# Kernel tuning notes

Hardware: AMD Instinct MI355X
Metric: run time of the kernel (lower is better)

## Reference

```python
import jax, jax.numpy as jnp
import numpy as np

N_NODES = 100000
K_HOPS = 10
ALPHA = 0.1


def gcn_conv(x, src, dst, W, b, num_nodes):
    # GCNConv: linear first (cheaper: out_dim small), then D^-1/2 (A+I) D^-1/2 aggregation
    h = x @ W  # [N, out]
    deg = jax.ops.segment_sum(jnp.ones_like(dst, dtype=h.dtype), dst, num_segments=num_nodes)
    dinv = jnp.where(deg > 0, jax.lax.rsqrt(deg), 0.0)
    norm = dinv[src] * dinv[dst]  # [E]
    msg = h[src] * norm[:, None]
    out = jax.ops.segment_sum(msg, dst, num_segments=num_nodes)
    return out + b


def _with_self_loops(edge_index, num_nodes):
    loops = jnp.arange(num_nodes, dtype=edge_index.dtype)
    src = jnp.concatenate([edge_index[0], loops])
    dst = jnp.concatenate([edge_index[1], loops])
    return src, dst


def setup_inputs() -> dict:
    key = jax.random.key(0)
    ks = jax.random.split(key, 8)
    n_feat, hidden, n_cls, n_edges = 512, 16, 7, 3200000
    x = jax.random.normal(ks[0], (N_NODES, n_feat), dtype=jnp.float32)
    edge_index = jax.random.randint(ks[1], (2, n_edges), 0, N_NODES, dtype=jnp.int64)
    W1 = jax.random.normal(ks[2], (n_feat, hidden), dtype=jnp.float32) * 0.05
    b1 = jnp.zeros((hidden,), dtype=jnp.float32)
    Wl = jax.random.normal(ks[3], (hidden, hidden), dtype=jnp.float32) * 0.25
    bl = jnp.zeros((hidden,), dtype=jnp.float32)
    W2 = jax.random.normal(ks[4], (hidden, n_cls), dtype=jnp.float32) * 0.25
    b2 = jnp.zeros((n_cls,), dtype=jnp.float32)
    return {"x": x, "edge_index": edge_index, "W1": W1, "b1": b1, "Wl": Wl, "bl": bl, "W2": W2, "b2": b2}


def reference(x, edge_index, W1, b1, Wl, bl, W2, b2):
    src, dst = _with_self_loops(edge_index, N_NODES)
    h = jax.nn.relu(gcn_conv(x, src, dst, W1, b1, N_NODES))
    def body(h, _):
        h = ALPHA * jax.nn.relu(h @ Wl + bl) + (1.0 - ALPHA) * h
        return h, None
    h, _ = jax.lax.scan(body, h, None, length=K_HOPS)
    out = gcn_conv(h, src, dst, W2, b2, N_NODES)
    return jax.nn.log_softmax(out, axis=1)
```

## Files before the change

### kernel.cpp

```cpp
#include <hip/hip_runtime.h>
#include <math.h>

#define N_NODES 100000
#define N_EDGES 3200000
#define F_IN    512
#define HID     16
#define NCLS    7
#define ALPHA   0.1f
#define K_HOPS  10

#define SHIFT   7
#define BWIDTH  128
#define NBUCK   ((N_NODES + BWIDTH - 1) / BWIDTH)
#define CHUNK   4096
#define BIN_T   512
#define EPT     (CHUNK / BIN_T)
#define A3_BLOCKS ((N_EDGES + CHUNK - 1) / CHUNK)

#define OFF_BCNT    0u
#define OFF_BSTART  1024u
#define OFF_BCUR    2048u
#define OFF_RP      3072u
#define OFF_DINV    103424u
#define OFF_COL     203776u
#define OFF_BINNED  3403776u
#define OFF_H0      6603776u
#define OFF_H1      8203776u
#define OFF_Z       9803776u

__global__ void k_bhist(const int* __restrict__ dst, int* __restrict__ bcnt) {
    __shared__ int h[NBUCK];
    int tid = threadIdx.x;
    for (int i = tid; i < NBUCK; i += 256) h[i] = 0;
    __syncthreads();
    for (int e = blockIdx.x * 256 + tid; e < N_EDGES; e += gridDim.x * 256)
        atomicAdd(&h[dst[e] >> SHIFT], 1);
    __syncthreads();
    for (int i = tid; i < NBUCK; i += 256) {
        int v = h[i];
        if (v) atomicAdd(&bcnt[i], v);
    }
}

__global__ void k_bscan(const int* __restrict__ bcnt, int* __restrict__ bstart,
                        int* __restrict__ bcur) {
    __shared__ int s[1024];
    int tid = threadIdx.x;
    int v = (tid < NBUCK) ? bcnt[tid] : 0;
    s[tid] = v;
    __syncthreads();
    for (int off = 1; off < 1024; off <<= 1) {
        int t = (tid >= off) ? s[tid - off] : 0;
        __syncthreads();
        s[tid] += t;
        __syncthreads();
    }
    if (tid < NBUCK) {
        int ex = s[tid] - v;
        bstart[tid] = ex;
        bcur[tid] = ex;
    }
    if (tid == 0) bstart[NBUCK] = N_EDGES;
}

__global__ void __launch_bounds__(BIN_T)
k_bin(const int* __restrict__ src, const int* __restrict__ dst,
      int* __restrict__ bcur, unsigned int* __restrict__ binned) {
    __shared__ int ha[NBUCK];
    __shared__ int gbase[NBUCK];
    __shared__ int lcur[NBUCK];
    int tid = threadIdx.x;
    int e0 = blockIdx.x * CHUNK;
    int e1 = e0 + CHUNK;
    if (e1 > N_EDGES) e1 = N_EDGES;
    for (int i = tid; i < NBUCK; i += BIN_T) ha[i] = 0;
    __syncthreads();
    int dloc[EPT];
#pragma unroll
    for (int i = 0; i < EPT; i++) {
        int e = e0 + tid + i * BIN_T;
        dloc[i] = (e < e1) ? dst[e] : -1;
        if (dloc[i] >= 0) atomicAdd(&ha[dloc[i] >> SHIFT], 1);
    }
    __syncthreads();
    for (int s = tid; s < NBUCK; s += BIN_T) {
        int c = ha[s];
        lcur[s] = 0;
        gbase[s] = c ? atomicAdd(&bcur[s], c) : 0;
    }
    __syncthreads();
#pragma unroll
    for (int i = 0; i < EPT; i++) {
        int d = dloc[i];
        if (d >= 0) {
            int e = e0 + tid + i * BIN_T;
            int bk = d >> SHIFT;
            int idx = atomicAdd(&lcur[bk], 1);
            binned[gbase[bk] + idx] =
                ((unsigned int)(d & (BWIDTH - 1)) << 17) | (unsigned int)src[e];
        }
    }
}

__global__ void __launch_bounds__(512)
k_csr(const unsigned int* __restrict__ binned, const int* __restrict__ bstart,
      int* __restrict__ rp, float* __restrict__ dinv, int* __restrict__ col) {
    __shared__ int cnt[BWIDTH];
    __shared__ int s[BWIDTH];
    __shared__ int cur[BWIDTH];
    int tid = threadIdx.x;
    int b = blockIdx.x;
    int base = b << SHIFT;
    int e0 = bstart[b], e1 = bstart[b + 1];
    if (tid < BWIDTH) cnt[tid] = 0;
    __syncthreads();
    for (int e = e0 + tid; e < e1; e += 512)
        atomicAdd(&cnt[binned[e] >> 17], 1);
    __syncthreads();
    int v = 0;
    if (tid < BWIDTH) { v = cnt[tid]; s[tid] = v; }
    __syncthreads();
    for (int off = 1; off < BWIDTH; off <<= 1) {
        int t = 0;
        if (tid < BWIDTH && tid >= off) t = s[tid - off];
        __syncthreads();
        if (tid < BWIDTH) s[tid] += t;
        __syncthreads();
    }
    if (tid < BWIDTH) {
        int ex = s[tid] - v;
        cur[tid] = ex;
        int node = base + tid;
        if (node < N_NODES) {
            rp[node] = e0 + ex;
            dinv[node] = rsqrtf((float)(v + 1));
        }
    }
    if (b == 0 && tid == 0) rp[N_NODES] = N_EDGES;
    __syncthreads();
    for (int e = e0 + tid; e < e1; e += 512) {
        unsigned int w = binned[e];
        int ln = (int)(w >> 17);
        int p = atomicAdd(&cur[ln], 1);
        col[e0 + p] = (int)(w & 0x1FFFFu);
    }
}

#define XW_ROWS 64
#define XW_KT   32
#define XW_S    36
#define XW_NT   (F_IN / XW_KT)
__global__ void k_xw1(const float* __restrict__ x, const float* __restrict__ W,
                      const float* __restrict__ dinv, float* __restrict__ h0s) {
    __shared__ float xT[2][XW_ROWS * XW_S];
    int tid = threadIdx.x;
    int rowBase = blockIdx.x * XW_ROWS;

    int rf0 = tid >> 3, kq = tid & 7;
    int rf1 = rf0 + 32;
    bool v0 = (rowBase + rf0) < N_NODES;
    bool v1 = (rowBase + rf1) < N_NODES;
    const float4* xrow0 = (const float4*)(x + (size_t)(rowBase + rf0) * F_IN);
    const float4* xrow1 = (const float4*)(x + (size_t)(rowBase + rf1) * F_IN);

    int r  = tid & 63;
    int cg = __builtin_amdgcn_readfirstlane(tid >> 6);
    const float4* W4 = (const float4*)W;

    float4 zero4 = make_float4(0.f, 0.f, 0.f, 0.f);
    float4 acc = zero4;
    float4 ld0 = v0 ? xrow0[kq] : zero4;
    float4 ld1 = v1 ? xrow1[kq] : zero4;

    for (int kt = 0; kt < XW_NT; kt++) {
        float* xb = xT[kt & 1];
        *(float4*)&xb[rf0 * XW_S + kq * 4] = ld0;
        *(float4*)&xb[rf1 * XW_S + kq * 4] = ld1;
        if (kt + 1 < XW_NT) {
            ld0 = v0 ? xrow0[(kt + 1) * 8 + kq] : zero4;
            ld1 = v1 ? xrow1[(kt + 1) * 8 + kq] : zero4;
        }
        __syncthreads();
        const float* xr = &xb[r * XW_S];
#pragma unroll
        for (int k8 = 0; k8 < 8; k8++) {
            float4 xv = *(const float4*)&xr[k8 * 4];
            float4 w0 = W4[(kt * XW_KT + k8 * 4 + 0) * 4 + cg];
            acc.x += xv.x * w0.x; acc.y += xv.x * w0.y;
            acc.z += xv.x * w0.z; acc.w += xv.x * w0.w;
            float4 w1 = W4[(kt * XW_KT + k8 * 4 + 1) * 4 + cg];
            acc.x += xv.y * w1.x; acc.y += xv.y * w1.y;
            acc.z += xv.y * w1.z; acc.w += xv.y * w1.w;
            float4 w2 = W4[(kt * XW_KT + k8 * 4 + 2) * 4 + cg];
            acc.x += xv.z * w2.x; acc.y += xv.z * w2.y;
            acc.z += xv.z * w2.z; acc.w += xv.z * w2.w;
            float4 w3 = W4[(kt * XW_KT + k8 * 4 + 3) * 4 + cg];
            acc.x += xv.w * w3.x; acc.y += xv.w * w3.y;
            acc.z += xv.w * w3.z; acc.w += xv.w * w3.w;
        }
        __syncthreads();
    }
    int node = rowBase + r;
    if (node < N_NODES) {
        float dv = dinv[node];
        float4 o;
        o.x = dv * acc.x; o.y = dv * acc.y; o.z = dv * acc.z; o.w = dv * acc.w;
        ((float4*)h0s)[(size_t)node * 4 + cg] = o;
    }
}

__global__ void k_agg1(const float* __restrict__ h0s, const int* __restrict__ rp,
                       const int* __restrict__ col, const float* __restrict__ dinv,
                       const float* __restrict__ b1, float* __restrict__ h1) {
    int node = (blockIdx.x * blockDim.x + threadIdx.x) >> 6;
    if (node >= N_NODES) return;
    int lane = threadIdx.x & 63;
    int c = lane & 15, eo = lane >> 4;
    int e0 = rp[node], e1 = rp[node + 1];
    float acc = 0.f;
    int e = e0 + eo;
    for (; e + 12 < e1; e += 16) {
        int c0 = col[e];
        int c1 = col[e + 4];
        int c2 = col[e + 8];
        int c3 = col[e + 12];
        float v0 = h0s[(size_t)c0 * HID + c];
        float v1 = h0s[(size_t)c1 * HID + c];
        float v2 = h0s[(size_t)c2 * HID + c];
        float v3 = h0s[(size_t)c3 * HID + c];
        acc += v0;
        acc += v1;
        acc += v2;
        acc += v3;
    }
    for (; e + 4 < e1; e += 8) {
        int c0 = col[e];
        int c1 = col[e + 4];
        float v0 = h0s[(size_t)c0 * HID + c];
        float v1 = h0s[(size_t)c1 * HID + c];
        acc += v0;
        acc += v1;
    }
    if (e < e1) acc += h0s[(size_t)col[e] * HID + c];
    acc += __shfl_xor(acc, 16);
    acc += __shfl_xor(acc, 32);
    float o = dinv[node] * (acc + h0s[(size_t)node * HID + c]) + b1[c];
    if (eo == 0) h1[(size_t)node * HID + c] = fmaxf(o, 0.f);
}

__global__ void k_hops(const float* __restrict__ h1, const float* __restrict__ Wl,
                       const float* __restrict__ bl, const float* __restrict__ W2,
                       const float* __restrict__ dinv, float* __restrict__ zs) {
    int node = blockIdx.x * blockDim.x + threadIdx.x;
    if (node >= N_NODES) return;
    float h[HID];
    const float4* h4 = (const float4*)(h1 + (size_t)node * HID);
#pragma unroll
    for (int q = 0; q < HID / 4; q++) {
        float4 v = h4[q];
        h[q * 4 + 0] = v.x; h[q * 4 + 1] = v.y;
        h[q * 4 + 2] = v.z; h[q * 4 + 3] = v.w;
    }
    for (int it = 0; it < K_HOPS; it++) {
        float tm[HID];
#pragma unroll
        for (int c = 0; c < HID; c++) tm[c] = bl[c];
#pragma unroll
        for (int k = 0; k < HID; k++) {
            float hk = h[k];
#pragma unroll
            for (int c = 0; c < HID; c++) tm[c] += hk * Wl[k * HID + c];
        }
#pragma unroll
        for (int c = 0; c < HID; c++)
            h[c] = ALPHA * fmaxf(tm[c], 0.f) + (1.f - ALPHA) * h[c];
    }
    float dv = dinv[node];
    float zz[8];
#pragma unroll
    for (int c = 0; c < 8; c++) zz[c] = 0.f;
#pragma unroll
    for (int k = 0; k < HID; k++) {
        float hk = h[k];
#pragma unroll
        for (int c = 0; c < NCLS; c++) zz[c] += hk * W2[k * NCLS + c];
    }
    float4* z4 = (float4*)(zs + (size_t)node * 8);
    float4 v0, v1;
    v0.x = dv * zz[0]; v0.y = dv * zz[1]; v0.z = dv * zz[2]; v0.w = dv * zz[3];
    v1.x = dv * zz[4]; v1.y = dv * zz[5]; v1.z = dv * zz[6]; v1.w = 0.f;
    z4[0] = v0; z4[1] = v1;
}

__global__ void k_agg2(const float* __restrict__ zs, const int* __restrict__ rp,
                       const int* __restrict__ col, const float* __restrict__ dinv,
                       const float* __restrict__ b2, float* __restrict__ out) {
    int node = (blockIdx.x * blockDim.x + threadIdx.x) >> 6;
    if (node >= N_NODES) return;
    int lane = threadIdx.x & 63;
    int c = lane & 7, eo = lane >> 3;
    int e0 = rp[node], e1 = rp[node + 1];
    float acc = 0.f;
    int e = e0 + eo;
    for (; e + 24 < e1; e += 32) {
        int c0 = col[e];
        int c1 = col[e + 8];
        int c2 = col[e + 16];
        int c3 = col[e + 24];
        float v0 = zs[(size_t)c0 * 8 + c];
        float v1 = zs[(size_t)c1 * 8 + c];
        float v2 = zs[(size_t)c2 * 8 + c];
        float v3 = zs[(size_t)c3 * 8 + c];
        acc += v0;
        acc += v1;
        acc += v2;
        acc += v3;
    }
    for (; e + 8 < e1; e += 16) {
        int c0 = col[e];
        int c1 = col[e + 8];
        float v0 = zs[(size_t)c0 * 8 + c];
        float v1 = zs[(size_t)c1 * 8 + c];
        acc += v0;
        acc += v1;
    }
    if (e < e1) acc += zs[(size_t)col[e] * 8 + c];
    acc += __shfl_xor(acc, 8);
    acc += __shfl_xor(acc, 16);
    acc += __shfl_xor(acc, 32);
    float o = dinv[node] * (acc + zs[(size_t)node * 8 + c]) + ((c < NCLS) ? b2[c] : 0.f);
    float val = (c < NCLS) ? o : -INFINITY;
    float m = val;
    m = fmaxf(m, __shfl_xor(m, 1));
    m = fmaxf(m, __shfl_xor(m, 2));
    m = fmaxf(m, __shfl_xor(m, 4));
    float ex = (c < NCLS) ? expf(o - m) : 0.f;
    float ss = ex;
    ss += __shfl_xor(ss, 1);
    ss += __shfl_xor(ss, 2);
    ss += __shfl_xor(ss, 4);
    if (eo == 0 && c < NCLS) out[(size_t)node * NCLS + c] = o - m - logf(ss);
}

extern "C" void kernel_launch(void* const* d_in, const int* in_sizes, int n_in,
                              void* d_out, int out_size, void* d_ws, size_t ws_size,
                              hipStream_t stream) {
    const float* x  = (const float*)d_in[0];
    const int*   ei = (const int*)d_in[1];
    const float* W1 = (const float*)d_in[2];
    const float* b1 = (const float*)d_in[3];
    const float* Wl = (const float*)d_in[4];
    const float* bl = (const float*)d_in[5];
    const float* W2 = (const float*)d_in[6];
    const float* b2 = (const float*)d_in[7];
    float* out = (float*)d_out;

    int*   wsI = (int*)d_ws;
    float* wsF = (float*)d_ws;
    int*          bcnt   = wsI + OFF_BCNT;
    int*          bstart = wsI + OFF_BSTART;
    int*          bcur   = wsI + OFF_BCUR;
    int*          rp     = wsI + OFF_RP;
    float*        dinv   = wsF + OFF_DINV;
    int*          col    = wsI + OFF_COL;
    unsigned int* binned = (unsigned int*)(wsI + OFF_BINNED);
    float*        h0s    = wsF + OFF_H0;
    float*        h1     = wsF + OFF_H1;
    float*        zs     = wsF + OFF_Z;

    const int* src = ei;
    const int* dst = ei + N_EDGES;

    hipMemsetAsync(bcnt, 0, NBUCK * sizeof(int), stream);

    k_bhist<<<1024, 256, 0, stream>>>(dst, bcnt);
    k_bscan<<<1, 1024, 0, stream>>>(bcnt, bstart, bcur);
    k_bin<<<A3_BLOCKS, BIN_T, 0, stream>>>(src, dst, bcur, binned);
    k_csr<<<NBUCK, 512, 0, stream>>>(binned, bstart, rp, dinv, col);
    k_xw1<<<(N_NODES + XW_ROWS - 1) / XW_ROWS, 256, 0, stream>>>(x, W1, dinv, h0s);
    k_agg1<<<(N_NODES * 64 + 255) / 256, 256, 0, stream>>>(h0s, rp, col, dinv, b1, h1);
    k_hops<<<(N_NODES + 255) / 256, 256, 0, stream>>>(h1, Wl, bl, W2, dinv, zs);
    k_agg2<<<(N_NODES * 64 + 255) / 256, 256, 0, stream>>>(zs, rp, col, dinv, b2, out);
}
```

Before: 568.0 us.

## Fuse all stages into one persistent kernel with grid-wide barriers

Merges the eight launches (histogram, scan, binning, CSR build, XW1, two aggregations, hops) into a single persistent kernel of 1024 blocks. Stages are separated by a software grid barrier built on global atomics and spin-waiting. The goal is to remove per-launch overhead and idle tails between the small kernels. The cost is barrier latency and grid-stride loops in place of full grids, plus a deadlock risk if the 1024 blocks cannot all be resident at once.

```diff
diff --git a/kernel.cpp b/kernel.cpp
--- a/kernel.cpp
+++ b/kernel.cpp
@@ -11,335 +11,375 @@
 
 #define SHIFT   7
 #define BWIDTH  128
-#define NBUCK   ((N_NODES + BWIDTH - 1) / BWIDTH)
-#define CHUNK   4096
-#define BIN_T   512
-#define EPT     (CHUNK / BIN_T)
-#define A3_BLOCKS ((N_EDGES + CHUNK - 1) / CHUNK)
-
-#define OFF_BCNT    0u
-#define OFF_BSTART  1024u
-#define OFF_BCUR    2048u
-#define OFF_RP      3072u
-#define OFF_DINV    103424u
-#define OFF_COL     203776u
-#define OFF_BINNED  3403776u
-#define OFF_H0      6603776u
-#define OFF_H1      8203776u
-#define OFF_Z       9803776u
-
-__global__ void k_bhist(const int* __restrict__ dst, int* __restrict__ bcnt) {
-    __shared__ int h[NBUCK];
-    int tid = threadIdx.x;
-    for (int i = tid; i < NBUCK; i += 256) h[i] = 0;
-    __syncthreads();
-    for (int e = blockIdx.x * 256 + tid; e < N_EDGES; e += gridDim.x * 256)
-        atomicAdd(&h[dst[e] >> SHIFT], 1);
-    __syncthreads();
-    for (int i = tid; i < NBUCK; i += 256) {
-        int v = h[i];
-        if (v) atomicAdd(&bcnt[i], v);
-    }
-}
-
-__global__ void k_bscan(const int* __restrict__ bcnt, int* __restrict__ bstart,
-                        int* __restrict__ bcur) {
-    __shared__ int s[1024];
-    int tid = threadIdx.x;
-    int v = (tid < NBUCK) ? bcnt[tid] : 0;
-    s[tid] = v;
-    __syncthreads();
-    for (int off = 1; off < 1024; off <<= 1) {
-        int t = (tid >= off) ? s[tid - off] : 0;
-        __syncthreads();
-        s[tid] += t;
-        __syncthreads();
-    }
-    if (tid < NBUCK) {
-        int ex = s[tid] - v;
-        bstart[tid] = ex;
-        bcur[tid] = ex;
-    }
-    if (tid == 0) bstart[NBUCK] = N_EDGES;
-}
-
-__global__ void __launch_bounds__(BIN_T)
-k_bin(const int* __restrict__ src, const int* __restrict__ dst,
-      int* __restrict__ bcur, unsigned int* __restrict__ binned) {
-    __shared__ int ha[NBUCK];
-    __shared__ int gbase[NBUCK];
-    __shared__ int lcur[NBUCK];
-    int tid = threadIdx.x;
-    int e0 = blockIdx.x * CHUNK;
-    int e1 = e0 + CHUNK;
-    if (e1 > N_EDGES) e1 = N_EDGES;
-    for (int i = tid; i < NBUCK; i += BIN_T) ha[i] = 0;
-    __syncthreads();
-    int dloc[EPT];
-#pragma unroll
-    for (int i = 0; i < EPT; i++) {
-        int e = e0 + tid + i * BIN_T;
-        dloc[i] = (e < e1) ? dst[e] : -1;
-        if (dloc[i] >= 0) atomicAdd(&ha[dloc[i] >> SHIFT], 1);
-    }
-    __syncthreads();
-    for (int s = tid; s < NBUCK; s += BIN_T) {
-        int c = ha[s];
-        lcur[s] = 0;
-        gbase[s] = c ? atomicAdd(&bcur[s], c) : 0;
-    }
-    __syncthreads();
-#pragma unroll
-    for (int i = 0; i < EPT; i++) {
-        int d = dloc[i];
-        if (d >= 0) {
-            int e = e0 + tid + i * BIN_T;
-            int bk = d >> SHIFT;
-            int idx = atomicAdd(&lcur[bk], 1);
-            binned[gbase[bk] + idx] =
-                ((unsigned int)(d & (BWIDTH - 1)) << 17) | (unsigned int)src[e];
-        }
-    }
-}
-
-__global__ void __launch_bounds__(512)
-k_csr(const unsigned int* __restrict__ binned, const int* __restrict__ bstart,
-      int* __restrict__ rp, float* __restrict__ dinv, int* __restrict__ col) {
-    __shared__ int cnt[BWIDTH];
-    __shared__ int s[BWIDTH];
-    __shared__ int cur[BWIDTH];
-    int tid = threadIdx.x;
-    int b = blockIdx.x;
-    int base = b << SHIFT;
-    int e0 = bstart[b], e1 = bstart[b + 1];
-    if (tid < BWIDTH) cnt[tid] = 0;
-    __syncthreads();
-    for (int e = e0 + tid; e < e1; e += 512)
-        atomicAdd(&cnt[binned[e] >> 17], 1);
-    __syncthreads();
-    int v = 0;
-    if (tid < BWIDTH) { v = cnt[tid]; s[tid] = v; }
-    __syncthreads();
-    for (int off = 1; off < BWIDTH; off <<= 1) {
-        int t = 0;
-        if (tid < BWIDTH && tid >= off) t = s[tid - off];
-        __syncthreads();
-        if (tid < BWIDTH) s[tid] += t;
-        __syncthreads();
-    }
-    if (tid < BWIDTH) {
-        int ex = s[tid] - v;
-        cur[tid] = ex;
-        int node = base + tid;
-        if (node < N_NODES) {
-            rp[node] = e0 + ex;
-            dinv[node] = rsqrtf((float)(v + 1));
-        }
-    }
-    if (b == 0 && tid == 0) rp[N_NODES] = N_EDGES;
-    __syncthreads();
-    for (int e = e0 + tid; e < e1; e += 512) {
-        unsigned int w = binned[e];
-        int ln = (int)(w >> 17);
-        int p = atomicAdd(&cur[ln], 1);
-        col[e0 + p] = (int)(w & 0x1FFFFu);
-    }
-}
+#define NBUCK   782
+#define CHUNK   2048
+#define EPT     8
+#define NCHUNK  ((N_EDGES + CHUNK - 1) / CHUNK)
+
+#define NB      1024
+#define BT      256
+#define NWAVES  (NB * (BT / 64))
+
+#define OFF_BAR     0u
+#define OFF_BCNT    1024u
+#define OFF_BSTART  2048u
+#define OFF_BCUR    3072u
+#define OFF_RP      4096u
+#define OFF_DINV    104448u
+#define OFF_COL     204800u
+#define OFF_BINNED  3404800u
+#define OFF_H0      6604800u
+#define OFF_H1      8204800u
+#define OFF_Z       9804800u
 
 #define XW_ROWS 64
 #define XW_KT   32
 #define XW_S    36
 #define XW_NT   (F_IN / XW_KT)
-__global__ void k_xw1(const float* __restrict__ x, const float* __restrict__ W,
-                      const float* __restrict__ dinv, float* __restrict__ h0s) {
-    __shared__ float xT[2][XW_ROWS * XW_S];
+#define XW_TILES ((N_NODES + XW_ROWS - 1) / XW_ROWS)
+
+__device__ __forceinline__ void gsync(int* bar, int idx) {
+    __syncthreads();
+    if (threadIdx.x == 0) {
+        __threadfence();
+        atomicAdd(&bar[idx], 1);
+        while (__hip_atomic_load(&bar[idx], __ATOMIC_RELAXED,
+                                 __HIP_MEMORY_SCOPE_AGENT) < NB)
+            __builtin_amdgcn_s_sleep(2);
+    }
+    __syncthreads();
+    __threadfence();
+}
+
+__global__ void __launch_bounds__(BT, 4)
+k_fused(const float* __restrict__ x, const int* __restrict__ src,
+        const int* __restrict__ dst,
+        const float* __restrict__ W1, const float* __restrict__ b1,
+        const float* __restrict__ Wl, const float* __restrict__ bl,
+        const float* __restrict__ W2, const float* __restrict__ b2,
+        int* __restrict__ bar, int* __restrict__ bcnt,
+        int* __restrict__ bstart, int* __restrict__ bcur,
+        int* __restrict__ rp, float* __restrict__ dinv,
+        int* __restrict__ col, unsigned int* __restrict__ binned,
+        float* __restrict__ h0s, float* __restrict__ h1,
+        float* __restrict__ zs, float* __restrict__ out) {
+    __shared__ __align__(16) int smem[4608];
     int tid = threadIdx.x;
-    int rowBase = blockIdx.x * XW_ROWS;
-
-    int rf0 = tid >> 3, kq = tid & 7;
-    int rf1 = rf0 + 32;
-    bool v0 = (rowBase + rf0) < N_NODES;
-    bool v1 = (rowBase + rf1) < N_NODES;
-    const float4* xrow0 = (const float4*)(x + (size_t)(rowBase + rf0) * F_IN);
-    const float4* xrow1 = (const float4*)(x + (size_t)(rowBase + rf1) * F_IN);
-
-    int r  = tid & 63;
-    int cg = __builtin_amdgcn_readfirstlane(tid >> 6);
-    const float4* W4 = (const float4*)W;
-
-    float4 zero4 = make_float4(0.f, 0.f, 0.f, 0.f);
-    float4 acc = zero4;
-    float4 ld0 = v0 ? xrow0[kq] : zero4;
-    float4 ld1 = v1 ? xrow1[kq] : zero4;
-
-    for (int kt = 0; kt < XW_NT; kt++) {
-        float* xb = xT[kt & 1];
-        *(float4*)&xb[rf0 * XW_S + kq * 4] = ld0;
-        *(float4*)&xb[rf1 * XW_S + kq * 4] = ld1;
-        if (kt + 1 < XW_NT) {
-            ld0 = v0 ? xrow0[(kt + 1) * 8 + kq] : zero4;
-            ld1 = v1 ? xrow1[(kt + 1) * 8 + kq] : zero4;
-        }
+
+    {
+        int* h = smem;
+        for (int i = tid; i < NBUCK; i += BT) h[i] = 0;
         __syncthreads();
-        const float* xr = &xb[r * XW_S];
-#pragma unroll
-        for (int k8 = 0; k8 < 8; k8++) {
-            float4 xv = *(const float4*)&xr[k8 * 4];
-            float4 w0 = W4[(kt * XW_KT + k8 * 4 + 0) * 4 + cg];
-            acc.x += xv.x * w0.x; acc.y += xv.x * w0.y;
-            acc.z += xv.x * w0.z; acc.w += xv.x * w0.w;
-            float4 w1 = W4[(kt * XW_KT + k8 * 4 + 1) * 4 + cg];
-            acc.x += xv.y * w1.x; acc.y += xv.y * w1.y;
-            acc.z += xv.y * w1.z; acc.w += xv.y * w1.w;
-            float4 w2 = W4[(kt * XW_KT + k8 * 4 + 2) * 4 + cg];
-            acc.x += xv.z * w2.x; acc.y += xv.z * w2.y;
-            acc.z += xv.z * w2.z; acc.w += xv.z * w2.w;
-            float4 w3 = W4[(kt * XW_KT + k8 * 4 + 3) * 4 + cg];
-            acc.x += xv.w * w3.x; acc.y += xv.w * w3.y;
-            acc.z += xv.w * w3.z; acc.w += xv.w * w3.w;
-        }
+        for (int e = blockIdx.x * BT + tid; e < N_EDGES; e += NB * BT)
+            atomicAdd(&h[dst[e] >> SHIFT], 1);
         __syncthreads();
-    }
-    int node = rowBase + r;
-    if (node < N_NODES) {
-        float dv = dinv[node];
-        float4 o;
-        o.x = dv * acc.x; o.y = dv * acc.y; o.z = dv * acc.z; o.w = dv * acc.w;
-        ((float4*)h0s)[(size_t)node * 4 + cg] = o;
-    }
-}
-
-__global__ void k_agg1(const float* __restrict__ h0s, const int* __restrict__ rp,
-                       const int* __restrict__ col, const float* __restrict__ dinv,
-                       const float* __restrict__ b1, float* __restrict__ h1) {
-    int node = (blockIdx.x * blockDim.x + threadIdx.x) >> 6;
-    if (node >= N_NODES) return;
-    int lane = threadIdx.x & 63;
-    int c = lane & 15, eo = lane >> 4;
-    int e0 = rp[node], e1 = rp[node + 1];
-    float acc = 0.f;
-    int e = e0 + eo;
-    for (; e + 12 < e1; e += 16) {
-        int c0 = col[e];
-        int c1 = col[e + 4];
-        int c2 = col[e + 8];
-        int c3 = col[e + 12];
-        float v0 = h0s[(size_t)c0 * HID + c];
-        float v1 = h0s[(size_t)c1 * HID + c];
-        float v2 = h0s[(size_t)c2 * HID + c];
-        float v3 = h0s[(size_t)c3 * HID + c];
-        acc += v0;
-        acc += v1;
-        acc += v2;
-        acc += v3;
-    }
-    for (; e + 4 < e1; e += 8) {
-        int c0 = col[e];
-        int c1 = col[e + 4];
-        float v0 = h0s[(size_t)c0 * HID + c];
-        float v1 = h0s[(size_t)c1 * HID + c];
-        acc += v0;
-        acc += v1;
-    }
-    if (e < e1) acc += h0s[(size_t)col[e] * HID + c];
-    acc += __shfl_xor(acc, 16);
-    acc += __shfl_xor(acc, 32);
-    float o = dinv[node] * (acc + h0s[(size_t)node * HID + c]) + b1[c];
-    if (eo == 0) h1[(size_t)node * HID + c] = fmaxf(o, 0.f);
-}
-
-__global__ void k_hops(const float* __restrict__ h1, const float* __restrict__ Wl,
-                       const float* __restrict__ bl, const float* __restrict__ W2,
-                       const float* __restrict__ dinv, float* __restrict__ zs) {
-    int node = blockIdx.x * blockDim.x + threadIdx.x;
-    if (node >= N_NODES) return;
-    float h[HID];
-    const float4* h4 = (const float4*)(h1 + (size_t)node * HID);
-#pragma unroll
-    for (int q = 0; q < HID / 4; q++) {
-        float4 v = h4[q];
-        h[q * 4 + 0] = v.x; h[q * 4 + 1] = v.y;
-        h[q * 4 + 2] = v.z; h[q * 4 + 3] = v.w;
-    }
-    for (int it = 0; it < K_HOPS; it++) {
-        float tm[HID];
-#pragma unroll
-        for (int c = 0; c < HID; c++) tm[c] = bl[c];
-#pragma unroll
-        for (int k = 0; k < HID; k++) {
-            float hk = h[k];
-#pragma unroll
-            for (int c = 0; c < HID; c++) tm[c] += hk * Wl[k * HID + c];
-        }
-#pragma unroll
-        for (int c = 0; c < HID; c++)
-            h[c] = ALPHA * fmaxf(tm[c], 0.f) + (1.f - ALPHA) * h[c];
-    }
-    float dv = dinv[node];
-    float zz[8];
-#pragma unroll
-    for (int c = 0; c < 8; c++) zz[c] = 0.f;
-#pragma unroll
-    for (int k = 0; k < HID; k++) {
-        float hk = h[k];
-#pragma unroll
-        for (int c = 0; c < NCLS; c++) zz[c] += hk * W2[k * NCLS + c];
-    }
-    float4* z4 = (float4*)(zs + (size_t)node * 8);
-    float4 v0, v1;
-    v0.x = dv * zz[0]; v0.y = dv * zz[1]; v0.z = dv * zz[2]; v0.w = dv * zz[3];
-    v1.x = dv * zz[4]; v1.y = dv * zz[5]; v1.z = dv * zz[6]; v1.w = 0.f;
-    z4[0] = v0; z4[1] = v1;
-}
-
-__global__ void k_agg2(const float* __restrict__ zs, const int* __restrict__ rp,
-                       const int* __restrict__ col, const float* __restrict__ dinv,
-                       const float* __restrict__ b2, float* __restrict__ out) {
-    int node = (blockIdx.x * blockDim.x + threadIdx.x) >> 6;
-    if (node >= N_NODES) return;
-    int lane = threadIdx.x & 63;
-    int c = lane & 7, eo = lane >> 3;
-    int e0 = rp[node], e1 = rp[node + 1];
-    float acc = 0.f;
-    int e = e0 + eo;
-    for (; e + 24 < e1; e += 32) {
-        int c0 = col[e];
-        int c1 = col[e + 8];
-        int c2 = col[e + 16];
-        int c3 = col[e + 24];
-        float v0 = zs[(size_t)c0 * 8 + c];
-        float v1 = zs[(size_t)c1 * 8 + c];
-        float v2 = zs[(size_t)c2 * 8 + c];
-        float v3 = zs[(size_t)c3 * 8 + c];
-        acc += v0;
-        acc += v1;
-        acc += v2;
-        acc += v3;
-    }
-    for (; e + 8 < e1; e += 16) {
-        int c0 = col[e];
-        int c1 = col[e + 8];
-        float v0 = zs[(size_t)c0 * 8 + c];
-        float v1 = zs[(size_t)c1 * 8 + c];
-        acc += v0;
-        acc += v1;
-    }
-    if (e < e1) acc += zs[(size_t)col[e] * 8 + c];
-    acc += __shfl_xor(acc, 8);
-    acc += __shfl_xor(acc, 16);
-    acc += __shfl_xor(acc, 32);
-    float o = dinv[node] * (acc + zs[(size_t)node * 8 + c]) + ((c < NCLS) ? b2[c] : 0.f);
-    float val = (c < NCLS) ? o : -INFINITY;
-    float m = val;
-    m = fmaxf(m, __shfl_xor(m, 1));
-    m = fmaxf(m, __shfl_xor(m, 2));
-    m = fmaxf(m, __shfl_xor(m, 4));
-    float ex = (c < NCLS) ? expf(o - m) : 0.f;
-    float ss = ex;
-    ss += __shfl_xor(ss, 1);
-    ss += __shfl_xor(ss, 2);
-    ss += __shfl_xor(ss, 4);
-    if (eo == 0 && c < NCLS) out[(size_t)node * NCLS + c] = o - m - logf(ss);
+        for (int i = tid; i < NBUCK; i += BT) {
+            int v = h[i];
+            if (v) atomicAdd(&bcnt[i], v);
+        }
+    }
+    gsync(bar, 0);
+
+    if (blockIdx.x == 0) {
+        int* s0 = smem;
+        int* s1 = smem + 1024;
+        for (int j = tid; j < 1024; j += BT) s0[j] = (j < NBUCK) ? bcnt[j] : 0;
+        __syncthreads();
+        int cur = 0;
+        for (int off = 1; off < 1024; off <<= 1) {
+            int* a = cur ? s1 : s0;
+            int* b = cur ? s0 : s1;
+            for (int j = tid; j < 1024; j += BT)
+                b[j] = a[j] + ((j >= off) ? a[j - off] : 0);
+            __syncthreads();
+            cur ^= 1;
+        }
+        int* a = cur ? s1 : s0;
+        for (int j = tid; j < 1024; j += BT) {
+            if (j < NBUCK) {
+                int ex = a[j] - bcnt[j];
+                bstart[j] = ex;
+                bcur[j] = ex;
+            }
+        }
+        if (tid == 0) bstart[NBUCK] = N_EDGES;
+    }
+    gsync(bar, 1);
+
+    {
+        int* ha    = smem;
+        int* gbase = smem + NBUCK;
+        int* lcur  = smem + 2 * NBUCK;
+        for (int ch = blockIdx.x; ch < NCHUNK; ch += NB) {
+            int e0 = ch * CHUNK;
+            int e1 = e0 + CHUNK;
+            if (e1 > N_EDGES) e1 = N_EDGES;
+            for (int i = tid; i < NBUCK; i += BT) ha[i] = 0;
+            __syncthreads();
+            int dloc[EPT];
+#pragma unroll
+            for (int i = 0; i < EPT; i++) {
+                int e = e0 + tid + i * BT;
+                dloc[i] = (e < e1) ? dst[e] : -1;
+                if (dloc[i] >= 0) atomicAdd(&ha[dloc[i] >> SHIFT], 1);
+            }
+            __syncthreads();
+            for (int s = tid; s < NBUCK; s += BT) {
+                int c = ha[s];
+                lcur[s] = 0;
+                gbase[s] = c ? atomicAdd(&bcur[s], c) : 0;
+            }
+            __syncthreads();
+#pragma unroll
+            for (int i = 0; i < EPT; i++) {
+                int d = dloc[i];
+                if (d >= 0) {
+                    int e = e0 + tid + i * BT;
+                    int bk = d >> SHIFT;
+                    int idx = atomicAdd(&lcur[bk], 1);
+                    binned[gbase[bk] + idx] =
+                        ((unsigned int)(d & (BWIDTH - 1)) << 17) | (unsigned int)src[e];
+                }
+            }
+            __syncthreads();
+        }
+    }
+    gsync(bar, 2);
+
+    {
+        int* cnt = smem;
+        int* s   = smem + BWIDTH;
+        int* cur = smem + 2 * BWIDTH;
+        for (int b = blockIdx.x; b < NBUCK; b += NB) {
+            int base = b << SHIFT;
+            int e0 = bstart[b], e1 = bstart[b + 1];
+            if (tid < BWIDTH) cnt[tid] = 0;
+            __syncthreads();
+            for (int e = e0 + tid; e < e1; e += BT)
+                atomicAdd(&cnt[binned[e] >> 17], 1);
+            __syncthreads();
+            int v = 0;
+            if (tid < BWIDTH) { v = cnt[tid]; s[tid] = v; }
+            __syncthreads();
+            for (int off = 1; off < BWIDTH; off <<= 1) {
+                int t = 0;
+                if (tid < BWIDTH && tid >= off) t = s[tid - off];
+                __syncthreads();
+                if (tid < BWIDTH) s[tid] += t;
+                __syncthreads();
+            }
+            if (tid < BWIDTH) {
+                int ex = s[tid] - v;
+                cur[tid] = ex;
+                int node = base + tid;
+                if (node < N_NODES) {
+                    rp[node] = e0 + ex;
+                    dinv[node] = rsqrtf((float)(v + 1));
+                }
+            }
+            if (b == 0 && tid == 0) rp[N_NODES] = N_EDGES;
+            __syncthreads();
+            for (int e = e0 + tid; e < e1; e += BT) {
+                unsigned int w = binned[e];
+                int ln = (int)(w >> 17);
+                int p = atomicAdd(&cur[ln], 1);
+                col[e0 + p] = (int)(w & 0x1FFFFu);
+            }
+            __syncthreads();
+        }
+    }
+    gsync(bar, 3);
+
+    {
+        float* xT = (float*)smem;
+        int rf0 = tid >> 3, kq = tid & 7;
+        int rf1 = rf0 + 32;
+        int r  = tid & 63;
+        int cg = __builtin_amdgcn_readfirstlane(tid >> 6);
+        const float4* W4 = (const float4*)W1;
+        float4 zero4 = make_float4(0.f, 0.f, 0.f, 0.f);
+
+        for (int t = blockIdx.x; t < XW_TILES; t += NB) {
+            int rowBase = t * XW_ROWS;
+            bool v0 = (rowBase + rf0) < N_NODES;
+            bool v1 = (rowBase + rf1) < N_NODES;
+            const float4* xrow0 = (const float4*)(x + (size_t)(rowBase + rf0) * F_IN);
+            const float4* xrow1 = (const float4*)(x + (size_t)(rowBase + rf1) * F_IN);
+            float4 acc = zero4;
+            float4 ld0 = v0 ? xrow0[kq] : zero4;
+            float4 ld1 = v1 ? xrow1[kq] : zero4;
+
+            for (int kt = 0; kt < XW_NT; kt++) {
+                float* xb = xT + (kt & 1) * (XW_ROWS * XW_S);
+                *(float4*)&xb[rf0 * XW_S + kq * 4] = ld0;
+                *(float4*)&xb[rf1 * XW_S + kq * 4] = ld1;
+                if (kt + 1 < XW_NT) {
+                    ld0 = v0 ? xrow0[(kt + 1) * 8 + kq] : zero4;
+                    ld1 = v1 ? xrow1[(kt + 1) * 8 + kq] : zero4;
+                }
+                __syncthreads();
+                const float* xr = &xb[r * XW_S];
+#pragma unroll
+                for (int k8 = 0; k8 < 8; k8++) {
+                    float4 xv = *(const float4*)&xr[k8 * 4];
+                    float4 w0 = W4[(kt * XW_KT + k8 * 4 + 0) * 4 + cg];
+                    acc.x += xv.x * w0.x; acc.y += xv.x * w0.y;
+                    acc.z += xv.x * w0.z; acc.w += xv.x * w0.w;
+                    float4 w1 = W4[(kt * XW_KT + k8 * 4 + 1) * 4 + cg];
+                    acc.x += xv.y * w1.x; acc.y += xv.y * w1.y;
+                    acc.z += xv.y * w1.z; acc.w += xv.y * w1.w;
+                    float4 w2 = W4[(kt * XW_KT + k8 * 4 + 2) * 4 + cg];
+                    acc.x += xv.z * w2.x; acc.y += xv.z * w2.y;
+                    acc.z += xv.z * w2.z; acc.w += xv.z * w2.w;
+                    float4 w3 = W4[(kt * XW_KT + k8 * 4 + 3) * 4 + cg];
+                    acc.x += xv.w * w3.x; acc.y += xv.w * w3.y;
+                    acc.z += xv.w * w3.z; acc.w += xv.w * w3.w;
+                }
+                __syncthreads();
+            }
+            int node = rowBase + r;
+            if (node < N_NODES) {
+                float dv = dinv[node];
+                float4 o;
+                o.x = dv * acc.x; o.y = dv * acc.y;
+                o.z = dv * acc.z; o.w = dv * acc.w;
+                ((float4*)h0s)[(size_t)node * 4 + cg] = o;
+            }
+        }
+    }
+    gsync(bar, 4);
+
+    {
+        int wid = blockIdx.x * (BT / 64) + (tid >> 6);
+        int lane = tid & 63;
+        int c = lane & 15, eo = lane >> 4;
+        for (int node = wid; node < N_NODES; node += NWAVES) {
+            int e0 = rp[node], e1 = rp[node + 1];
+            float acc = 0.f;
+            int e = e0 + eo;
+            for (; e + 12 < e1; e += 16) {
+                int c0 = col[e];
+                int c1 = col[e + 4];
+                int c2 = col[e + 8];
+                int c3 = col[e + 12];
+                float v0 = h0s[(size_t)c0 * HID + c];
+                float v1 = h0s[(size_t)c1 * HID + c];
+                float v2 = h0s[(size_t)c2 * HID + c];
+                float v3 = h0s[(size_t)c3 * HID + c];
+                acc += v0;
+                acc += v1;
+                acc += v2;
+                acc += v3;
+            }
+            for (; e + 4 < e1; e += 8) {
+                int c0 = col[e];
+                int c1 = col[e + 4];
+                float v0 = h0s[(size_t)c0 * HID + c];
+                float v1 = h0s[(size_t)c1 * HID + c];
+                acc += v0;
+                acc += v1;
+            }
+            if (e < e1) acc += h0s[(size_t)col[e] * HID + c];
+            acc += __shfl_xor(acc, 16);
+            acc += __shfl_xor(acc, 32);
+            float o = dinv[node] * (acc + h0s[(size_t)node * HID + c]) + b1[c];
+            if (eo == 0) h1[(size_t)node * HID + c] = fmaxf(o, 0.f);
+        }
+    }
+    gsync(bar, 5);
+
+    {
+        for (int node = blockIdx.x * BT + tid; node < N_NODES; node += NB * BT) {
+            float h[HID];
+            const float4* h4 = (const float4*)(h1 + (size_t)node * HID);
+#pragma unroll
+            for (int q = 0; q < HID / 4; q++) {
+                float4 v = h4[q];
+                h[q * 4 + 0] = v.x; h[q * 4 + 1] = v.y;
+                h[q * 4 + 2] = v.z; h[q * 4 + 3] = v.w;
+            }
+            for (int it = 0; it < K_HOPS; it++) {
+                float tm[HID];
+#pragma unroll
+                for (int cc = 0; cc < HID; cc++) tm[cc] = bl[cc];
+#pragma unroll
+                for (int k = 0; k < HID; k++) {
+                    float hk = h[k];
+#pragma unroll
+                    for (int cc = 0; cc < HID; cc++) tm[cc] += hk * Wl[k * HID + cc];
+                }
+#pragma unroll
+                for (int cc = 0; cc < HID; cc++)
+                    h[cc] = ALPHA * fmaxf(tm[cc], 0.f) + (1.f - ALPHA) * h[cc];
+            }
+            float dv = dinv[node];
+            float zz[8];
+#pragma unroll
+            for (int cc = 0; cc < 8; cc++) zz[cc] = 0.f;
+#pragma unroll
+            for (int k = 0; k < HID; k++) {
+                float hk = h[k];
+#pragma unroll
+                for (int cc = 0; cc < NCLS; cc++) zz[cc] += hk * W2[k * NCLS + cc];
+            }
+            float4* z4 = (float4*)(zs + (size_t)node * 8);
+            float4 v0, v1;
+            v0.x = dv * zz[0]; v0.y = dv * zz[1]; v0.z = dv * zz[2]; v0.w = dv * zz[3];
+            v1.x = dv * zz[4]; v1.y = dv * zz[5]; v1.z = dv * zz[6]; v1.w = 0.f;
+            z4[0] = v0; z4[1] = v1;
+        }
+    }
+    gsync(bar, 6);
+
+    {
+        int wid = blockIdx.x * (BT / 64) + (tid >> 6);
+        int lane = tid & 63;
+        int c = lane & 7, eo = lane >> 3;
+        for (int node = wid; node < N_NODES; node += NWAVES) {
+            int e0 = rp[node], e1 = rp[node + 1];
+            float acc = 0.f;
+            int e = e0 + eo;
+            for (; e + 24 < e1; e += 32) {
+                int c0 = col[e];
+                int c1 = col[e + 8];
+                int c2 = col[e + 16];
+                int c3 = col[e + 24];
+                float v0 = zs[(size_t)c0 * 8 + c];
+                float v1 = zs[(size_t)c1 * 8 + c];
+                float v2 = zs[(size_t)c2 * 8 + c];
+                float v3 = zs[(size_t)c3 * 8 + c];
+                acc += v0;
+                acc += v1;
+                acc += v2;
+                acc += v3;
+            }
+            for (; e + 8 < e1; e += 16) {
+                int c0 = col[e];
+                int c1 = col[e + 8];
+                float v0 = zs[(size_t)c0 * 8 + c];
+                float v1 = zs[(size_t)c1 * 8 + c];
+                acc += v0;
+                acc += v1;
+            }
+            if (e < e1) acc += zs[(size_t)col[e] * 8 + c];
+            acc += __shfl_xor(acc, 8);
+            acc += __shfl_xor(acc, 16);
+            acc += __shfl_xor(acc, 32);
+            float o = dinv[node] * (acc + zs[(size_t)node * 8 + c])
+                      + ((c < NCLS) ? b2[c] : 0.f);
+            float val = (c < NCLS) ? o : -INFINITY;
+            float m = val;
+            m = fmaxf(m, __shfl_xor(m, 1));
+            m = fmaxf(m, __shfl_xor(m, 2));
+            m = fmaxf(m, __shfl_xor(m, 4));
+            float ex = (c < NCLS) ? expf(o - m) : 0.f;
+            float ss = ex;
+            ss += __shfl_xor(ss, 1);
+            ss += __shfl_xor(ss, 2);
+            ss += __shfl_xor(ss, 4);
+            if (eo == 0 && c < NCLS) out[(size_t)node * NCLS + c] = o - m - logf(ss);
+        }
+    }
 }
 
 extern "C" void kernel_launch(void* const* d_in, const int* in_sizes, int n_in,
@@ -357,6 +397,7 @@
 
     int*   wsI = (int*)d_ws;
     float* wsF = (float*)d_ws;
+    int*          bar    = wsI + OFF_BAR;
     int*          bcnt   = wsI + OFF_BCNT;
     int*          bstart = wsI + OFF_BSTART;
     int*          bcur   = wsI + OFF_BCUR;
@@ -371,14 +412,9 @@
     const int* src = ei;
     const int* dst = ei + N_EDGES;
 
-    hipMemsetAsync(bcnt, 0, NBUCK * sizeof(int), stream);
-
-    k_bhist<<<1024, 256, 0, stream>>>(dst, bcnt);
-    k_bscan<<<1, 1024, 0, stream>>>(bcnt, bstart, bcur);
-    k_bin<<<A3_BLOCKS, BIN_T, 0, stream>>>(src, dst, bcur, binned);
-    k_csr<<<NBUCK, 512, 0, stream>>>(binned, bstart, rp, dinv, col);
-    k_xw1<<<(N_NODES + XW_ROWS - 1) / XW_ROWS, 256, 0, stream>>>(x, W1, dinv, h0s);
-    k_agg1<<<(N_NODES * 64 + 255) / 256, 256, 0, stream>>>(h0s, rp, col, dinv, b1, h1);
-    k_hops<<<(N_NODES + 255) / 256, 256, 0, stream>>>(h1, Wl, bl, W2, dinv, zs);
-    k_agg2<<<(N_NODES * 64 + 255) / 256, 256, 0, stream>>>(zs, rp, col, dinv, b2, out);
+    hipMemsetAsync(wsI, 0, (OFF_BCNT + NBUCK) * sizeof(int), stream);
+
+    k_fused<<<NB, BT, 0, stream>>>(x, src, dst, W1, b1, Wl, bl, W2, b2,
+                                   bar, bcnt, bstart, bcur, rp, dinv,
+                                   col, binned, h0s, h1, zs, out);
 }
```

After: 1.724 ms. +203.6%, slower.

## Rewrite x@W1 as persistent wave-per-row kernel with register-resident weights

Applied to the files above, without the earlier changes.

The x@W1 GEMV is restructured so each wavefront handles one node row at a time. Each lane keeps an 8x16 slice of W1 in registers and loads 8 contiguous floats of the row, and a butterfly shuffle reduction produces the 16 outputs. A grid-stride persistent loop with next-row prefetch replaces the shared-memory tiled version, removing LDS traffic and barriers. The cost is 128 weight registers per lane, which may lower occupancy, plus the shuffle overhead.

```diff
diff --git a/kernel.cpp b/kernel.cpp
--- a/kernel.cpp
+++ b/kernel.cpp
@@ -146,66 +146,105 @@
     }
 }
 
-#define XW_ROWS 64
-#define XW_KT   32
-#define XW_S    36
-#define XW_NT   (F_IN / XW_KT)
-__global__ void k_xw1(const float* __restrict__ x, const float* __restrict__ W,
-                      const float* __restrict__ dinv, float* __restrict__ h0s) {
-    __shared__ float xT[2][XW_ROWS * XW_S];
-    int tid = threadIdx.x;
-    int rowBase = blockIdx.x * XW_ROWS;
-
-    int rf0 = tid >> 3, kq = tid & 7;
-    int rf1 = rf0 + 32;
-    bool v0 = (rowBase + rf0) < N_NODES;
-    bool v1 = (rowBase + rf1) < N_NODES;
-    const float4* xrow0 = (const float4*)(x + (size_t)(rowBase + rf0) * F_IN);
-    const float4* xrow1 = (const float4*)(x + (size_t)(rowBase + rf1) * F_IN);
-
-    int r  = tid & 63;
-    int cg = __builtin_amdgcn_readfirstlane(tid >> 6);
+#define XWN_BLOCKS 512
+#define XWN_WAVES  (XWN_BLOCKS * 4)
+
+__device__ __forceinline__ float4 shfl4_xor(float4 v, int m) {
+    float4 r;
+    r.x = __shfl_xor(v.x, m);
+    r.y = __shfl_xor(v.y, m);
+    r.z = __shfl_xor(v.z, m);
+    r.w = __shfl_xor(v.w, m);
+    return r;
+}
+__device__ __forceinline__ float4 add4(float4 a, float4 b) {
+    a.x += b.x; a.y += b.y; a.z += b.z; a.w += b.w;
+    return a;
+}
+
+__global__ void __launch_bounds__(256)
+k_xw1(const float* __restrict__ x, const float* __restrict__ W,
+      const float* __restrict__ dinv, float* __restrict__ h0s) {
+    int lane = threadIdx.x & 63;
+    int wid = (blockIdx.x * 256 + threadIdx.x) >> 6;
+
+    float4 w[32];
     const float4* W4 = (const float4*)W;
-
-    float4 zero4 = make_float4(0.f, 0.f, 0.f, 0.f);
-    float4 acc = zero4;
-    float4 ld0 = v0 ? xrow0[kq] : zero4;
-    float4 ld1 = v1 ? xrow1[kq] : zero4;
-
-    for (int kt = 0; kt < XW_NT; kt++) {
-        float* xb = xT[kt & 1];
-        *(float4*)&xb[rf0 * XW_S + kq * 4] = ld0;
-        *(float4*)&xb[rf1 * XW_S + kq * 4] = ld1;
-        if (kt + 1 < XW_NT) {
-            ld0 = v0 ? xrow0[(kt + 1) * 8 + kq] : zero4;
-            ld1 = v1 ? xrow1[(kt + 1) * 8 + kq] : zero4;
+#pragma unroll
+    for (int j = 0; j < 8; j++) {
+#pragma unroll
+        for (int q = 0; q < 4; q++)
+            w[j * 4 + q] = W4[(8 * lane + j) * 4 + q];
+    }
+
+    int node = wid;
+    const float4* xr0 = (const float4*)(x + (size_t)node * F_IN) + 2 * lane;
+    float4 xc0 = xr0[0];
+    float4 xc1 = xr0[1];
+
+    for (; node < N_NODES; node += XWN_WAVES) {
+        int nn = node + XWN_WAVES;
+        float4 xn0, xn1;
+        if (nn < N_NODES) {
+            const float4* xr = (const float4*)(x + (size_t)nn * F_IN) + 2 * lane;
+            xn0 = xr[0];
+            xn1 = xr[1];
         }
-        __syncthreads();
-        const float* xr = &xb[r * XW_S];
-#pragma unroll
-        for (int k8 = 0; k8 < 8; k8++) {
-            float4 xv = *(const float4*)&xr[k8 * 4];
-            float4 w0 = W4[(kt * XW_KT + k8 * 4 + 0) * 4 + cg];
-            acc.x += xv.x * w0.x; acc.y += xv.x * w0.y;
-            acc.z += xv.x * w0.z; acc.w += xv.x * w0.w;
-            float4 w1 = W4[(kt * XW_KT + k8 * 4 + 1) * 4 + cg];
-            acc.x += xv.y * w1.x; acc.y += xv.y * w1.y;
-            acc.z += xv.y * w1.z; acc.w += xv.y * w1.w;
-            float4 w2 = W4[(kt * XW_KT + k8 * 4 + 2) * 4 + cg];
-            acc.x += xv.z * w2.x; acc.y += xv.z * w2.y;
-            acc.z += xv.z * w2.z; acc.w += xv.z * w2.w;
-            float4 w3 = W4[(kt * XW_KT + k8 * 4 + 3) * 4 + cg];
-            acc.x += xv.w * w3.x; acc.y += xv.w * w3.y;
-            acc.z += xv.w * w3.z; acc.w += xv.w * w3.w;
+
+        float xa0 = xc0.x, xa1 = xc0.y, xa2 = xc0.z, xa3 = xc0.w;
+        float xa4 = xc1.x, xa5 = xc1.y, xa6 = xc1.z, xa7 = xc1.w;
+
+        float4 pp0 = make_float4(0.f, 0.f, 0.f, 0.f);
+        float4 pp1 = pp0, pp2 = pp0, pp3 = pp0;
+#define XW_FMA(J, XA)                                            \
+        pp0.x += XA * w[J*4+0].x; pp0.y += XA * w[J*4+0].y;      \
+        pp0.z += XA * w[J*4+0].z; pp0.w += XA * w[J*4+0].w;      \
+        pp1.x += XA * w[J*4+1].x; pp1.y += XA * w[J*4+1].y;      \
+        pp1.z += XA * w[J*4+1].z; pp1.w += XA * w[J*4+1].w;      \
+        pp2.x += XA * w[J*4+2].x; pp2.y += XA * w[J*4+2].y;      \
+        pp2.z += XA * w[J*4+2].z; pp2.w += XA * w[J*4+2].w;      \
+        pp3.x += XA * w[J*4+3].x; pp3.y += XA * w[J*4+3].y;      \
+        pp3.z += XA * w[J*4+3].z; pp3.w += XA * w[J*4+3].w;
+        XW_FMA(0, xa0) XW_FMA(1, xa1) XW_FMA(2, xa2) XW_FMA(3, xa3)
+        XW_FMA(4, xa4) XW_FMA(5, xa5) XW_FMA(6, xa6) XW_FMA(7, xa7)
+#undef XW_FMA
+
+        int b5 = (lane >> 5) & 1;
+        float4 k0 = b5 ? pp2 : pp0;
+        float4 k1 = b5 ? pp3 : pp1;
+        float4 s0 = b5 ? pp0 : pp2;
+        float4 s1 = b5 ? pp1 : pp3;
+        k0 = add4(k0, shfl4_xor(s0, 32));
+        k1 = add4(k1, shfl4_xor(s1, 32));
+
+        int b4 = (lane >> 4) & 1;
+        float4 kk = b4 ? k1 : k0;
+        float4 ss = b4 ? k0 : k1;
+        kk = add4(kk, shfl4_xor(ss, 16));
+
+        int b3 = (lane >> 3) & 1;
+        float e0 = b3 ? kk.z : kk.x;
+        float e1 = b3 ? kk.w : kk.y;
+        float f0 = b3 ? kk.x : kk.z;
+        float f1 = b3 ? kk.y : kk.w;
+        e0 += __shfl_xor(f0, 8);
+        e1 += __shfl_xor(f1, 8);
+
+        int b2 = (lane >> 2) & 1;
+        float v = b2 ? e1 : e0;
+        float sv = b2 ? e0 : e1;
+        v += __shfl_xor(sv, 4);
+
+        v += __shfl_xor(v, 1);
+        v += __shfl_xor(v, 2);
+
+        if ((lane & 3) == 0) {
+            float dv = dinv[node];
+            h0s[(size_t)node * HID + (lane >> 2)] = dv * v;
         }
-        __syncthreads();
-    }
-    int node = rowBase + r;
-    if (node < N_NODES) {
-        float dv = dinv[node];
-        float4 o;
-        o.x = dv * acc.x; o.y = dv * acc.y; o.z = dv * acc.z; o.w = dv * acc.w;
-        ((float4*)h0s)[(size_t)node * 4 + cg] = o;
+
+        xc0 = xn0;
+        xc1 = xn1;
     }
 }
 
@@ -377,7 +416,7 @@
     k_bscan<<<1, 1024, 0, stream>>>(bcnt, bstart, bcur);
     k_bin<<<A3_BLOCKS, BIN_T, 0, stream>>>(src, dst, bcur, binned);
     k_csr<<<NBUCK, 512, 0, stream>>>(binned, bstart, rp, dinv, col);
-    k_xw1<<<(N_NODES + XW_ROWS - 1) / XW_ROWS, 256, 0, stream>>>(x, W1, dinv, h0s);
+    k_xw1<<<XWN_BLOCKS, 256, 0, stream>>>(x, W1, dinv, h0s);
     k_agg1<<<(N_NODES * 64 + 255) / 256, 256, 0, stream>>>(h0s, rp, col, dinv, b1, h1);
     k_hops<<<(N_NODES + 255) / 256, 256, 0, stream>>>(h1, Wl, bl, W2, dinv, zs);
     k_agg2<<<(N_NODES * 64 + 255) / 256, 256, 0, stream>>>(zs, rp, col, dinv, b2, out);
```

Result: no change. 558.1 us (-1.7%).
